# Performance work log

Hardware: AMD Instinct MI355X
Metric: run time of the kernel (lower is better)

## Reference

```python
import jax, jax.numpy as jnp
import numpy as np

E, TOPK, HID, FFN = 8, 2, 1024, 2048  # experts, top_k, hidden K, intermediate N
B, S = 2, 1024


def setup_inputs() -> dict:
    key = jax.random.key(0)
    ks = jax.random.split(key, 7)
    return {
        "x": jax.random.normal(ks[0], (B, S, HID), jnp.float32),
        "router_weight": jax.random.normal(ks[1], (E, HID), jnp.float32) * 0.02,
        "router_bias": jax.random.normal(ks[2], (E,), jnp.float32) * 0.02,
        "w1": jax.random.normal(ks[3], (E, 2 * FFN, HID), jnp.float32) * 0.02,  # [E,2N,K] gate|up
        "w1_bias": jax.random.normal(ks[4], (E, 2 * FFN), jnp.float32) * 0.02,
        "w2": jax.random.normal(ks[5], (E, HID, FFN), jnp.float32) * 0.02,      # [E,K,N]
        "w2_bias": jax.random.normal(ks[6], (E, HID), jnp.float32) * 0.02,
        "top_k": TOPK,
    }


def reference(x, router_weight, router_bias, w1, w1_bias, w2, w2_bias, top_k):
    Bb, Ss, K = x.shape
    xf = x.reshape(-1, K)                                   # [M,K]
    M = xf.shape[0]
    Ne = w1.shape[0]
    # --- route_tokens: softmax over experts, then top-k (megablocks style) ---
    logits = xf @ router_weight.T + router_bias             # [M,E]
    probs = jax.nn.softmax(logits, axis=-1)
    topk_w, topk_ids = jax.lax.top_k(probs, top_k)          # [M,topk]
    # combine weights: scatter top-k probs into dense [M,E]
    comb = jnp.zeros((M, Ne), xf.dtype).at[jnp.arange(M)[:, None], topk_ids].add(topk_w)
    # --- fused experts (dense combine formulation, same math as grouped GEMM) ---
    gu = jnp.einsum('mk,enk->men', xf, w1) + w1_bias[None]  # [M,E,2N]
    Nf = gu.shape[-1] // 2
    gate, up = gu[..., :Nf], gu[..., Nf:]
    h = jax.nn.silu(gate) * up                              # silu_and_mul (SwiGLU)
    down = jnp.einsum('men,ekn->mek', h, w2) + w2_bias[None]  # [M,E,K]
    out = jnp.einsum('mek,me->mk', down, comb)              # weighted combine
    return out.reshape(Bb, Ss, K), topk_w
```

## Files before the change

kernel.cpp:

```cpp
#include <hip/hip_runtime.h>
#include <hip/hip_bf16.h>
#include <math.h>

#define E_    8
#define HID_  1024
#define FFN_  2048
#define M_    2048
#define NP_   (M_*2)

typedef __attribute__((ext_vector_type(8))) short bf16x8;
typedef __attribute__((ext_vector_type(4))) float f32x4;

typedef const __attribute__((address_space(1))) void GVOID;
typedef __attribute__((address_space(3))) void LVOID;

#define VMCNT4 asm volatile("s_waitcnt vmcnt(4)" ::: "memory")
#define VMCNT0 asm volatile("s_waitcnt vmcnt(0)" ::: "memory")

__device__ __forceinline__ short f2bf(float f) {
    union { __hip_bfloat16 b; short s; } u;
    u.b = __float2bfloat16(f);
    return u.s;
}

__global__ __launch_bounds__(256) void cvt_kernel(
    const float* __restrict__ src, __hip_bfloat16* __restrict__ dst, int n4)
{
    int stride = gridDim.x * 256;
    for (int i = blockIdx.x * 256 + threadIdx.x; i < n4; i += stride) {
        float4 v = ((const float4*)src)[i];
        short4 o;
        o.x = f2bf(v.x); o.y = f2bf(v.y); o.z = f2bf(v.z); o.w = f2bf(v.w);
        ((short4*)dst)[i] = o;
    }
}

__global__ __launch_bounds__(64) void router_kernel(
    const float* __restrict__ x, const float* __restrict__ rw,
    const float* __restrict__ rb, int* __restrict__ ids,
    float* __restrict__ wts, int* __restrict__ cnt,
    float* __restrict__ topk_out)
{
    const int m    = blockIdx.x;
    const int lane = threadIdx.x;
    const float4* xm4 = (const float4*)(x + (size_t)m * HID_);

    float4 xv[4];
#pragma unroll
    for (int j = 0; j < 4; ++j) xv[j] = xm4[j*64 + lane];

    float lg[E_];
#pragma unroll
    for (int e = 0; e < E_; ++e) {
        const float4* we4 = (const float4*)(rw + e * HID_);
        float s = 0.f;
#pragma unroll
        for (int j = 0; j < 4; ++j) {
            float4 w = we4[j*64 + lane];
            s = fmaf(xv[j].x, w.x, s);
            s = fmaf(xv[j].y, w.y, s);
            s = fmaf(xv[j].z, w.z, s);
            s = fmaf(xv[j].w, w.w, s);
        }
        lg[e] = s;
    }
#pragma unroll
    for (int off = 32; off; off >>= 1)
#pragma unroll
        for (int e = 0; e < E_; ++e) lg[e] += __shfl_xor(lg[e], off);

    if (lane == 0) {
        float l2[E_], p[E_];
        float mx = -1e30f;
#pragma unroll
        for (int e = 0; e < E_; ++e) { l2[e] = lg[e] + rb[e]; mx = fmaxf(mx, l2[e]); }
        float sum = 0.f;
#pragma unroll
        for (int e = 0; e < E_; ++e) { p[e] = expf(l2[e] - mx); sum += p[e]; }
        float inv = 1.f / sum;
#pragma unroll
        for (int e = 0; e < E_; ++e) p[e] *= inv;

        int   i1 = -1, i2 = -1;
        float v1 = -1e30f, v2 = -1e30f;
#pragma unroll
        for (int e = 0; e < E_; ++e) {
            float pe = p[e];
            if (pe > v1)      { v2 = v1; i2 = i1; v1 = pe; i1 = e; }
            else if (pe > v2) { v2 = pe; i2 = e; }
        }
        ids[2*m]   = i1;  ids[2*m+1]   = i2;
        wts[2*m]   = v1;  wts[2*m+1]   = v2;
        topk_out[2*m]   = v1;
        topk_out[2*m+1] = v2;
        atomicAdd(&cnt[i1], 1);
        atomicAdd(&cnt[i2], 1);
    }
}

__global__ void offsets_kernel(const int* __restrict__ cnt,
                               int* __restrict__ off, int* __restrict__ fill)
{
    if (threadIdx.x == 0 && blockIdx.x == 0) {
        int acc = 0;
        for (int e = 0; e < E_; ++e) { off[e] = acc; fill[e] = acc; acc += cnt[e]; }
    }
}

__global__ __launch_bounds__(256) void scatter_kernel(
    const int* __restrict__ ids, const float* __restrict__ wts,
    int* __restrict__ fill, int* __restrict__ gtok, float* __restrict__ gwt,
    int* __restrict__ pos)
{
    int m = blockIdx.x * 256 + threadIdx.x;
    if (m >= M_) return;
#pragma unroll
    for (int s = 0; s < 2; ++s) {
        int e = ids[2*m + s];
        int p = atomicAdd(&fill[e], 1);
        gtok[p] = m;
        gwt[p]  = wts[2*m + s];
        pos[2*m + s] = p;
    }
}


__global__ __launch_bounds__(256, 3) void gemm1_kernel(
    const __hip_bfloat16* __restrict__ xb, const __hip_bfloat16* __restrict__ w1bf,
    const float* __restrict__ w1b, const int* __restrict__ gtok,
    const int* __restrict__ cnt, const int* __restrict__ off,
    __hip_bfloat16* __restrict__ h)
{
    const int e  = blockIdx.z;
    const int ce = cnt[e];
    const int t0 = blockIdx.y * 128;
    if (t0 >= ce) return;
    const int n0   = blockIdx.x * 64;
    const int base = off[e];
    const __hip_bfloat16* w1e = w1bf + (size_t)e * (2*FFN_) * HID_;

    __shared__ __align__(16) __hip_bfloat16 As[3][128*32];
    __shared__ __align__(16) __hip_bfloat16 Bs[3][128*32];

    const int tid  = threadIdx.x;
    const int lane = tid & 63;
    const int wid  = tid >> 6;
    const int wm   = wid >> 1;
    const int wn   = wid & 1;

    const __hip_bfloat16 *asrc[2], *bsrc[2];
#pragma unroll
    for (int q = 0; q < 2; ++q) {
        int slot = q*256 + tid;
        int r = slot >> 2, p = slot & 3;
        int c = p ^ ((r >> 1) & 3);
        int rr  = min(t0 + r, ce - 1);
        asrc[q] = xb + (size_t)gtok[base + rr] * HID_ + c*8;
        int q2 = r >> 5, s = r & 31;
        int grow = (q2 & 1) ? (FFN_ + n0 + (q2>>1)*32 + s)
                            : (       n0 + (q2>>1)*32 + s);
        bsrc[q] = w1e + (size_t)grow * HID_ + c*8;
    }

    auto STAGE = [&](int b, int k0) {
#pragma unroll
        for (int q = 0; q < 2; ++q)
            __builtin_amdgcn_global_load_lds((GVOID*)(asrc[q] + k0),
                (LVOID*)(&As[b][(q*256 + wid*64)*8]), 16, 0, 0);
#pragma unroll
        for (int q = 0; q < 2; ++q)
            __builtin_amdgcn_global_load_lds((GVOID*)(bsrc[q] + k0),
                (LVOID*)(&Bs[b][(q*256 + wid*64)*8]), 16, 0, 0);
    };

    f32x4 acc[4][4];
#pragma unroll
    for (int m = 0; m < 4; ++m)
#pragma unroll
        for (int n = 0; n < 4; ++n) acc[m][n] = (f32x4){0.f,0.f,0.f,0.f};

    const int cf = lane >> 4;
    auto COMPUTE = [&](int cb) {
        bf16x8 af[4], bfr[4];
#pragma unroll
        for (int m = 0; m < 4; ++m) {
            int r = wm*64 + m*16 + (lane & 15);
            int sw = cf ^ ((r >> 1) & 3);
            af[m] = *(bf16x8*)&As[cb][r*32 + sw*8];
        }
#pragma unroll
        for (int n = 0; n < 4; ++n) {
            int r = wn*64 + n*16 + (lane & 15);
            int sw = cf ^ ((r >> 1) & 3);
            bfr[n] = *(bf16x8*)&Bs[cb][r*32 + sw*8];
        }
        __builtin_amdgcn_s_setprio(1);
#pragma unroll
        for (int m = 0; m < 4; ++m)
#pragma unroll
            for (int n = 0; n < 4; ++n)
                acc[m][n] = __builtin_amdgcn_mfma_f32_16x16x32_bf16(
                    af[m], bfr[n], acc[m][n], 0, 0, 0);
        __builtin_amdgcn_s_setprio(0);
    };

    const int NT = HID_/32;
    STAGE(0, 0);
    STAGE(1, 32);
    VMCNT4;
    __builtin_amdgcn_s_barrier();

    int cb = 0;
    for (int t = 0; t < NT-2; ++t) {
        int sb = cb + 2; if (sb >= 3) sb -= 3;
        STAGE(sb, (t+2)*32);
        COMPUTE(cb);
        VMCNT4;
        __builtin_amdgcn_s_barrier();
        if (++cb == 3) cb = 0;
    }
    COMPUTE(cb);
    VMCNT0;
    __builtin_amdgcn_s_barrier();
    if (++cb == 3) cb = 0;
    COMPUTE(cb);

    const float* w1be = w1b + e*2*FFN_;
#pragma unroll
    for (int n = 0; n < 2; ++n) {
        int col = n0 + wn*32 + n*16 + (lane & 15);
        float bg = w1be[col];
        float bu = w1be[FFN_ + col];
#pragma unroll
        for (int m = 0; m < 4; ++m) {
            int rb2 = t0 + wm*64 + m*16 + (lane >> 4)*4;
#pragma unroll
            for (int i = 0; i < 4; ++i) {
                int t = rb2 + i;
                if (t < ce) {
                    float g = acc[m][n][i]   + bg;
                    float u = acc[m][n+2][i] + bu;
                    float hv = (g / (1.f + __expf(-g))) * u;
                    h[(size_t)(base + t)*FFN_ + col] = __float2bfloat16(hv);
                }
            }
        }
    }
}

__global__ __launch_bounds__(256, 3) void gemm2_kernel(
    const __hip_bfloat16* __restrict__ h, const __hip_bfloat16* __restrict__ w2bf,
    const float* __restrict__ w2b, const float* __restrict__ gwt,
    const int* __restrict__ cnt, const int* __restrict__ off,
    float* __restrict__ dpair)
{
    const int e  = blockIdx.z & 7;
    const int ks = blockIdx.z >> 3;
    const int ce = cnt[e];
    const int t0 = blockIdx.y * 128;
    if (t0 >= ce) return;
    const int n0    = blockIdx.x * 128;
    const int base  = off[e];
    const int kbase = ks * (FFN_/2);
    const __hip_bfloat16* w2e = w2bf + (size_t)e * HID_ * FFN_;

    __shared__ __align__(16) __hip_bfloat16 As[3][128*32];
    __shared__ __align__(16) __hip_bfloat16 Bs[3][128*32];

    const int tid  = threadIdx.x;
    const int lane = tid & 63;
    const int wid  = tid >> 6;
    const int wm   = wid >> 1;
    const int wn   = wid & 1;

    const __hip_bfloat16 *asrc[2], *bsrc[2];
#pragma unroll
    for (int q = 0; q < 2; ++q) {
        int slot = q*256 + tid;
        int r = slot >> 2, p = slot & 3;
        int c = p ^ ((r >> 1) & 3);
        int rr = min(t0 + r, ce - 1);
        asrc[q] = h   + (size_t)(base + rr) * FFN_ + kbase + c*8;
        bsrc[q] = w2e + (size_t)(n0 + r)    * FFN_ + kbase + c*8;
    }

    auto STAGE = [&](int b, int k0) {
#pragma unroll
        for (int q = 0; q < 2; ++q)
            __builtin_amdgcn_global_load_lds((GVOID*)(asrc[q] + k0),
                (LVOID*)(&As[b][(q*256 + wid*64)*8]), 16, 0, 0);
#pragma unroll
        for (int q = 0; q < 2; ++q)
            __builtin_amdgcn_global_load_lds((GVOID*)(bsrc[q] + k0),
                (LVOID*)(&Bs[b][(q*256 + wid*64)*8]), 16, 0, 0);
    };

    f32x4 acc[4][4];
#pragma unroll
    for (int m = 0; m < 4; ++m)
#pragma unroll
        for (int n = 0; n < 4; ++n) acc[m][n] = (f32x4){0.f,0.f,0.f,0.f};

    const int cf = lane >> 4;
    auto COMPUTE = [&](int cb) {
        bf16x8 af[4], bfr[4];
#pragma unroll
        for (int m = 0; m < 4; ++m) {
            int r = wm*64 + m*16 + (lane & 15);
            int sw = cf ^ ((r >> 1) & 3);
            af[m] = *(bf16x8*)&As[cb][r*32 + sw*8];
        }
#pragma unroll
        for (int n = 0; n < 4; ++n) {
            int r = wn*64 + n*16 + (lane & 15);
            int sw = cf ^ ((r >> 1) & 3);
            bfr[n] = *(bf16x8*)&Bs[cb][r*32 + sw*8];
        }
        __builtin_amdgcn_s_setprio(1);
#pragma unroll
        for (int m = 0; m < 4; ++m)
#pragma unroll
            for (int n = 0; n < 4; ++n)
                acc[m][n] = __builtin_amdgcn_mfma_f32_16x16x32_bf16(
                    af[m], bfr[n], acc[m][n], 0, 0, 0);
        __builtin_amdgcn_s_setprio(0);
    };

    const int NT = (FFN_/2)/32;
    STAGE(0, 0);
    STAGE(1, 32);
    VMCNT4;
    __builtin_amdgcn_s_barrier();

    int cb = 0;
    for (int t = 0; t < NT-2; ++t) {
        int sb = cb + 2; if (sb >= 3) sb -= 3;
        STAGE(sb, (t+2)*32);
        COMPUTE(cb);
        VMCNT4;
        __builtin_amdgcn_s_barrier();
        if (++cb == 3) cb = 0;
    }
    COMPUTE(cb);
    VMCNT0;
    __builtin_amdgcn_s_barrier();
    if (++cb == 3) cb = 0;
    COMPUTE(cb);

    const float* w2be = w2b + e*HID_;
    float* dpk = dpair + (size_t)ks * NP_ * HID_;
#pragma unroll
    for (int n = 0; n < 4; ++n) {
        int col = n0 + wn*64 + n*16 + (lane & 15);
        float bias = (ks == 0) ? w2be[col] : 0.f;
#pragma unroll
        for (int m = 0; m < 4; ++m) {
            int rb2 = t0 + wm*64 + m*16 + (lane >> 4)*4;
#pragma unroll
            for (int i = 0; i < 4; ++i) {
                int t = rb2 + i;
                if (t < ce) {
                    int p   = base + t;
                    float w = gwt[p];
                    dpk[(size_t)p*HID_ + col] = w * (acc[m][n][i] + bias);
                }
            }
        }
    }
}

__global__ __launch_bounds__(256) void combine_kernel(
    const float* __restrict__ dpair, const int* __restrict__ pos,
    float* __restrict__ out)
{
    int idx = blockIdx.x * 256 + threadIdx.x;
    int m   = idx >> 8;
    int c4  = (idx & 255) * 4;
    int p0 = pos[2*m], p1 = pos[2*m+1];
    const float* d0 = dpair;
    const float* d1 = dpair + (size_t)NP_ * HID_;
    float4 a0 = *(const float4*)(d0 + (size_t)p0*HID_ + c4);
    float4 a1 = *(const float4*)(d1 + (size_t)p0*HID_ + c4);
    float4 b0 = *(const float4*)(d0 + (size_t)p1*HID_ + c4);
    float4 b1 = *(const float4*)(d1 + (size_t)p1*HID_ + c4);
    float4 o = make_float4((a0.x+a1.x)+(b0.x+b1.x), (a0.y+a1.y)+(b0.y+b1.y),
                           (a0.z+a1.z)+(b0.z+b1.z), (a0.w+a1.w)+(b0.w+b1.w));
    *(float4*)(out + (size_t)m*HID_ + c4) = o;
}

__global__ __launch_bounds__(256) void gemm1_rs_kernel(
    const __hip_bfloat16* __restrict__ xb, const float* __restrict__ w1,
    const float* __restrict__ w1b, const int* __restrict__ gtok,
    const int* __restrict__ cnt, const int* __restrict__ off,
    __hip_bfloat16* __restrict__ h)
{
    const int e  = blockIdx.z;
    const int ce = cnt[e];
    const int t0 = blockIdx.y * 128;
    if (t0 >= ce) return;
    const int n0   = blockIdx.x * 64;
    const int base = off[e];
    const float* w1e = w1 + (size_t)e * (2*FFN_) * HID_;

    __shared__ __align__(16) __hip_bfloat16 As[128*64];
    __shared__ __align__(16) __hip_bfloat16 Bs[128*64];

    const int tid  = threadIdx.x;
    const int lane = tid & 63;
    const int wid  = tid >> 6;
    const int wm   = wid >> 1;
    const int wn   = wid & 1;

    const __hip_bfloat16* asrc[4];
#pragma unroll
    for (int q = 0; q < 4; ++q) {
        int slot = q*256 + tid;
        int r = slot >> 3, p = slot & 7;
        int rr  = min(t0 + r, ce - 1);
        int tok = gtok[base + rr];
        int c = p ^ (r & 7);
        asrc[q] = xb + (size_t)tok * HID_ + c*8;
    }

    const int brow = tid >> 1;
    const int hk   = tid & 1;
    const int q2 = brow >> 5, s = brow & 31;
    const int grow = (q2 & 1) ? (FFN_ + n0 + (q2>>1)*32 + s)
                              : (       n0 + (q2>>1)*32 + s);
    const float* bsrc = w1e + (size_t)grow * HID_ + hk*32;

    f32x4 acc[4][4];
#pragma unroll
    for (int m = 0; m < 4; ++m)
#pragma unroll
        for (int n = 0; n < 4; ++n) acc[m][n] = (f32x4){0.f,0.f,0.f,0.f};

    float4 breg[8];
#pragma unroll
    for (int j = 0; j < 8; ++j) breg[j] = *(const float4*)(bsrc + j*4);

    for (int k0 = 0; k0 < HID_; k0 += 64) {
#pragma unroll
        for (int q = 0; q < 4; ++q) {
            __builtin_amdgcn_global_load_lds(
                (GVOID*)(asrc[q] + k0),
                (LVOID*)(&As[(q*256 + wid*64)*8]), 16, 0, 0);
        }
#pragma unroll
        for (int cc = 0; cc < 4; ++cc) {
            union { bf16x8 v; short s8[8]; } u;
            const float* f0 = (const float*)&breg[2*cc];
#pragma unroll
            for (int j = 0; j < 8; ++j) u.s8[j] = f2bf(f0[j]);
            int c = hk*4 + cc, p = c ^ (brow & 7);
            *(bf16x8*)&Bs[brow*64 + p*8] = u.v;
        }
        __syncthreads();

        if (k0 + 64 < HID_) {
#pragma unroll
            for (int j = 0; j < 8; ++j) breg[j] = *(const float4*)(bsrc + (k0+64) + j*4);
        }

        bf16x8 af[4][2], bfr[4][2];
#pragma unroll
        for (int m = 0; m < 4; ++m)
#pragma unroll
            for (int kk = 0; kk < 2; ++kk) {
                int r = wm*64 + m*16 + (lane & 15);
                int c = kk*4 + (lane >> 4), p = c ^ (r & 7);
                af[m][kk] = *(bf16x8*)&As[r*64 + p*8];
            }
#pragma unroll
        for (int n = 0; n < 4; ++n)
#pragma unroll
            for (int kk = 0; kk < 2; ++kk) {
                int r = wn*64 + n*16 + (lane & 15);
                int c = kk*4 + (lane >> 4), p = c ^ (r & 7);
                bfr[n][kk] = *(bf16x8*)&Bs[r*64 + p*8];
            }
#pragma unroll
        for (int kk = 0; kk < 2; ++kk)
#pragma unroll
            for (int m = 0; m < 4; ++m)
#pragma unroll
                for (int n = 0; n < 4; ++n)
                    acc[m][n] = __builtin_amdgcn_mfma_f32_16x16x32_bf16(
                        af[m][kk], bfr[n][kk], acc[m][n], 0, 0, 0);
        __syncthreads();
    }

    const float* w1be = w1b + e*2*FFN_;
#pragma unroll
    for (int n = 0; n < 2; ++n) {
        int col = n0 + wn*32 + n*16 + (lane & 15);
        float bg = w1be[col];
        float bu = w1be[FFN_ + col];
#pragma unroll
        for (int m = 0; m < 4; ++m) {
            int rb2 = t0 + wm*64 + m*16 + (lane >> 4)*4;
#pragma unroll
            for (int i = 0; i < 4; ++i) {
                int t = rb2 + i;
                if (t < ce) {
                    float g = acc[m][n][i]   + bg;
                    float u = acc[m][n+2][i] + bu;
                    float hv = (g / (1.f + __expf(-g))) * u;
                    h[(size_t)(base + t)*FFN_ + col] = __float2bfloat16(hv);
                }
            }
        }
    }
}

__global__ __launch_bounds__(256) void gemm2_rs_kernel(
    const __hip_bfloat16* __restrict__ h, const float* __restrict__ w2,
    const float* __restrict__ w2b, const int* __restrict__ gtok,
    const float* __restrict__ gwt, const int* __restrict__ cnt,
    const int* __restrict__ off, float* __restrict__ out)
{
    const int e  = blockIdx.z;
    const int ce = cnt[e];
    const int t0 = blockIdx.y * 128;
    if (t0 >= ce) return;
    const int n0   = blockIdx.x * 128;
    const int base = off[e];
    const float* w2e = w2 + (size_t)e * HID_ * FFN_;

    __shared__ __align__(16) __hip_bfloat16 As[128*64];
    __shared__ __align__(16) __hip_bfloat16 Bs[128*64];

    const int tid  = threadIdx.x;
    const int lane = tid & 63;
    const int wid  = tid >> 6;
    const int wm   = wid >> 1;
    const int wn   = wid & 1;

    const __hip_bfloat16* asrc[4];
#pragma unroll
    for (int q = 0; q < 4; ++q) {
        int slot = q*256 + tid;
        int r = slot >> 3, p = slot & 7;
        int rr = min(t0 + r, ce - 1);
        int c = p ^ (r & 7);
        asrc[q] = h + (size_t)(base + rr) * FFN_ + c*8;
    }

    const int brow = tid >> 1;
    const int hk   = tid & 1;
    const float* bsrc = w2e + (size_t)(n0 + brow) * FFN_ + hk*32;

    f32x4 acc[4][4];
#pragma unroll
    for (int m = 0; m < 4; ++m)
#pragma unroll
        for (int n = 0; n < 4; ++n) acc[m][n] = (f32x4){0.f,0.f,0.f,0.f};

    float4 breg[8];
#pragma unroll
    for (int j = 0; j < 8; ++j) breg[j] = *(const float4*)(bsrc + j*4);

    for (int k0 = 0; k0 < FFN_; k0 += 64) {
#pragma unroll
        for (int q = 0; q < 4; ++q) {
            __builtin_amdgcn_global_load_lds(
                (GVOID*)(asrc[q] + k0),
                (LVOID*)(&As[(q*256 + wid*64)*8]), 16, 0, 0);
        }
#pragma unroll
        for (int cc = 0; cc < 4; ++cc) {
            union { bf16x8 v; short s8[8]; } u;
            const float* f0 = (const float*)&breg[2*cc];
#pragma unroll
            for (int j = 0; j < 8; ++j) u.s8[j] = f2bf(f0[j]);
            int c = hk*4 + cc, p = c ^ (brow & 7);
            *(bf16x8*)&Bs[brow*64 + p*8] = u.v;
        }
        __syncthreads();

        if (k0 + 64 < FFN_) {
#pragma unroll
            for (int j = 0; j < 8; ++j) breg[j] = *(const float4*)(bsrc + (k0+64) + j*4);
        }

        bf16x8 af[4][2], bfr[4][2];
#pragma unroll
        for (int m = 0; m < 4; ++m)
#pragma unroll
            for (int kk = 0; kk < 2; ++kk) {
                int r = wm*64 + m*16 + (lane & 15);
                int c = kk*4 + (lane >> 4), p = c ^ (r & 7);
                af[m][kk] = *(bf16x8*)&As[r*64 + p*8];
            }
#pragma unroll
        for (int n = 0; n < 4; ++n)
#pragma unroll
            for (int kk = 0; kk < 2; ++kk) {
                int r = wn*64 + n*16 + (lane & 15);
                int c = kk*4 + (lane >> 4), p = c ^ (r & 7);
                bfr[n][kk] = *(bf16x8*)&Bs[r*64 + p*8];
            }
#pragma unroll
        for (int kk = 0; kk < 2; ++kk)
#pragma unroll
            for (int m = 0; m < 4; ++m)
#pragma unroll
                for (int n = 0; n < 4; ++n)
                    acc[m][n] = __builtin_amdgcn_mfma_f32_16x16x32_bf16(
                        af[m][kk], bfr[n][kk], acc[m][n], 0, 0, 0);
        __syncthreads();
    }

    const float* w2be = w2b + e*HID_;
#pragma unroll
    for (int n = 0; n < 4; ++n) {
        int col = n0 + wn*64 + n*16 + (lane & 15);
        float bias = w2be[col];
#pragma unroll
        for (int m = 0; m < 4; ++m) {
            int rb2 = t0 + wm*64 + m*16 + (lane >> 4)*4;
#pragma unroll
            for (int i = 0; i < 4; ++i) {
                int t = rb2 + i;
                if (t < ce) {
                    int p   = base + t;
                    float w = gwt[p];
                    atomicAdd(&out[(size_t)gtok[p]*HID_ + col], w * (acc[m][n][i] + bias));
                }
            }
        }
    }
}

extern "C" void kernel_launch(void* const* d_in, const int* in_sizes, int n_in,
                              void* d_out, int out_size, void* d_ws, size_t ws_size,
                              hipStream_t stream)
{
    const float* x   = (const float*)d_in[0];
    const float* rw  = (const float*)d_in[1];
    const float* rb  = (const float*)d_in[2];
    const float* w1  = (const float*)d_in[3];
    const float* w1b = (const float*)d_in[4];
    const float* w2  = (const float*)d_in[5];
    const float* w2b = (const float*)d_in[6];

    float* out      = (float*)d_out;
    float* topk_out = out + (size_t)M_ * HID_;

    char*  ws   = (char*)d_ws;
    int*   ids  = (int*)  (ws);
    float* wts  = (float*)(ws + 16384);
    int*   gtok = (int*)  (ws + 32768);
    float* gwt  = (float*)(ws + 49152);
    int*   cnt  = (int*)  (ws + 65536);
    int*   off  = (int*)  (ws + 65536 + 128);
    int*   fill = (int*)  (ws + 65536 + 256);
    int*   pos  = (int*)  (ws + 98304);

    const size_t MB = 1024*1024;
    __hip_bfloat16* xb    = (__hip_bfloat16*)(ws + 131072);
    __hip_bfloat16* h     = (__hip_bfloat16*)(ws + 131072 + 4*MB);
    float*          dpair = (float*)         (ws + 131072 + 20*MB);
    __hip_bfloat16* w1bf  = (__hip_bfloat16*)(ws + 131072 + 52*MB);
    __hip_bfloat16* w2bf  = (__hip_bfloat16*)(ws + 131072 + 116*MB);
    const bool tier2 = (ws_size >= 131072 + 148*MB);

    hipMemsetAsync(cnt, 0, E_ * sizeof(int), stream);

    cvt_kernel<<<2048, 256, 0, stream>>>(x, xb, (M_*HID_)/4);
    router_kernel<<<M_, 64, 0, stream>>>(x, rw, rb, ids, wts, cnt, topk_out);
    offsets_kernel<<<1, 64, 0, stream>>>(cnt, off, fill);
    scatter_kernel<<<M_/256, 256, 0, stream>>>(ids, wts, fill, gtok, gwt, pos);

    if (tier2) {
        cvt_kernel<<<4096, 256, 0, stream>>>(w1, w1bf, (E_*2*FFN_*HID_)/4);
        cvt_kernel<<<4096, 256, 0, stream>>>(w2, w2bf, (E_*HID_*FFN_)/4);

        dim3 g1(FFN_/64, M_/128, E_);
        gemm1_kernel<<<g1, 256, 0, stream>>>(xb, w1bf, w1b, gtok, cnt, off, h);

        dim3 g2(HID_/128, M_/128, 2*E_);
        gemm2_kernel<<<g2, 256, 0, stream>>>(h, w2bf, w2b, gwt, cnt, off, dpair);

        combine_kernel<<<(M_*HID_)/(256*4), 256, 0, stream>>>(dpair, pos, out);
    } else {
        hipMemsetAsync(out, 0, (size_t)M_ * HID_ * sizeof(float), stream);

        dim3 g1(FFN_/64, M_/128, E_);
        gemm1_rs_kernel<<<g1, 256, 0, stream>>>(xb, w1, w1b, gtok, cnt, off, h);

        dim3 g2(HID_/128, M_/128, E_);
        gemm2_rs_kernel<<<g2, 256, 0, stream>>>(h, w2, w2b, gtok, gwt, cnt, off, out);
    }
}
```

Before: 252.2 us.

## Fuse x bf16 conversion into router, merge weight casts, deepen GEMM pipeline

The activation fp32→bf16 conversion moves into the router kernel, which already loads x, so one launch and one read of x go away. The two weight-conversion launches merge into a single kernel. Both grouped GEMMs go from a 3-stage to a 4-stage LDS cp.async ring with vmcnt(8) waits, keeping more loads in flight. In exchange, launch bounds drop to 2 blocks per CU because of the larger shared-memory footprint, which may reduce occupancy.

```diff
diff --git a/kernel.cpp b/kernel.cpp
--- a/kernel.cpp
+++ b/kernel.cpp
@@ -14,6 +14,7 @@
 typedef const __attribute__((address_space(1))) void GVOID;
 typedef __attribute__((address_space(3))) void LVOID;
 
+#define VMCNT8 asm volatile("s_waitcnt vmcnt(8)" ::: "memory")
 #define VMCNT4 asm volatile("s_waitcnt vmcnt(4)" ::: "memory")
 #define VMCNT0 asm volatile("s_waitcnt vmcnt(0)" ::: "memory")
 
@@ -23,15 +24,21 @@
     return u.s;
 }
 
-__global__ __launch_bounds__(256) void cvt_kernel(
-    const float* __restrict__ src, __hip_bfloat16* __restrict__ dst, int n4)
-{
+__global__ __launch_bounds__(256) void cvt_w_kernel(
+    const float* __restrict__ w1, const float* __restrict__ w2,
+    __hip_bfloat16* __restrict__ w1bf, __hip_bfloat16* __restrict__ w2bf)
+{
+    const int n1 = (E_*2*FFN_*HID_)/4;
+    const int n2 = (E_*HID_*FFN_)/4;
     int stride = gridDim.x * 256;
-    for (int i = blockIdx.x * 256 + threadIdx.x; i < n4; i += stride) {
-        float4 v = ((const float4*)src)[i];
+    for (int i = blockIdx.x * 256 + threadIdx.x; i < n1 + n2; i += stride) {
+        float4 v;
+        if (i < n1) v = ((const float4*)w1)[i];
+        else        v = ((const float4*)w2)[i - n1];
         short4 o;
         o.x = f2bf(v.x); o.y = f2bf(v.y); o.z = f2bf(v.z); o.w = f2bf(v.w);
-        ((short4*)dst)[i] = o;
+        if (i < n1) ((short4*)w1bf)[i] = o;
+        else        ((short4*)w2bf)[i - n1] = o;
     }
 }
 
@@ -39,7 +46,7 @@
     const float* __restrict__ x, const float* __restrict__ rw,
     const float* __restrict__ rb, int* __restrict__ ids,
     float* __restrict__ wts, int* __restrict__ cnt,
-    float* __restrict__ topk_out)
+    float* __restrict__ topk_out, __hip_bfloat16* __restrict__ xb)
 {
     const int m    = blockIdx.x;
     const int lane = threadIdx.x;
@@ -48,6 +55,15 @@
     float4 xv[4];
 #pragma unroll
     for (int j = 0; j < 4; ++j) xv[j] = xm4[j*64 + lane];
+
+    short4* xbr = (short4*)(xb + (size_t)m * HID_);
+#pragma unroll
+    for (int j = 0; j < 4; ++j) {
+        short4 o;
+        o.x = f2bf(xv[j].x); o.y = f2bf(xv[j].y);
+        o.z = f2bf(xv[j].z); o.w = f2bf(xv[j].w);
+        xbr[j*64 + lane] = o;
+    }
 
     float lg[E_];
 #pragma unroll
@@ -125,7 +141,7 @@
 }
 
 
-__global__ __launch_bounds__(256, 3) void gemm1_kernel(
+__global__ __launch_bounds__(256, 2) void gemm1_kernel(
     const __hip_bfloat16* __restrict__ xb, const __hip_bfloat16* __restrict__ w1bf,
     const float* __restrict__ w1b, const int* __restrict__ gtok,
     const int* __restrict__ cnt, const int* __restrict__ off,
@@ -139,14 +155,15 @@
     const int base = off[e];
     const __hip_bfloat16* w1e = w1bf + (size_t)e * (2*FFN_) * HID_;
 
-    __shared__ __align__(16) __hip_bfloat16 As[3][128*32];
-    __shared__ __align__(16) __hip_bfloat16 Bs[3][128*32];
+    __shared__ __align__(16) __hip_bfloat16 As[4][128*32];
+    __shared__ __align__(16) __hip_bfloat16 Bs[4][128*32];
 
     const int tid  = threadIdx.x;
     const int lane = tid & 63;
     const int wid  = tid >> 6;
     const int wm   = wid >> 1;
     const int wn   = wid & 1;
+    const int cf   = lane >> 4;
 
     const __hip_bfloat16 *asrc[2], *bsrc[2];
 #pragma unroll
@@ -179,7 +196,6 @@
 #pragma unroll
         for (int n = 0; n < 4; ++n) acc[m][n] = (f32x4){0.f,0.f,0.f,0.f};
 
-    const int cf = lane >> 4;
     auto COMPUTE = [&](int cb) {
         bf16x8 af[4], bfr[4];
 #pragma unroll
@@ -207,23 +223,23 @@
     const int NT = HID_/32;
     STAGE(0, 0);
     STAGE(1, 32);
+    STAGE(2, 64);
+    VMCNT8;
+    __builtin_amdgcn_s_barrier();
+
+    for (int t = 0; t < NT-3; ++t) {
+        STAGE((t+3) & 3, (t+3)*32);
+        COMPUTE(t & 3);
+        VMCNT8;
+        __builtin_amdgcn_s_barrier();
+    }
+    COMPUTE((NT-3) & 3);
     VMCNT4;
     __builtin_amdgcn_s_barrier();
-
-    int cb = 0;
-    for (int t = 0; t < NT-2; ++t) {
-        int sb = cb + 2; if (sb >= 3) sb -= 3;
-        STAGE(sb, (t+2)*32);
-        COMPUTE(cb);
-        VMCNT4;
-        __builtin_amdgcn_s_barrier();
-        if (++cb == 3) cb = 0;
-    }
-    COMPUTE(cb);
+    COMPUTE((NT-2) & 3);
     VMCNT0;
     __builtin_amdgcn_s_barrier();
-    if (++cb == 3) cb = 0;
-    COMPUTE(cb);
+    COMPUTE((NT-1) & 3);
 
     const float* w1be = w1b + e*2*FFN_;
 #pragma unroll
@@ -248,7 +264,7 @@
     }
 }
 
-__global__ __launch_bounds__(256, 3) void gemm2_kernel(
+__global__ __launch_bounds__(256, 2) void gemm2_kernel(
     const __hip_bfloat16* __restrict__ h, const __hip_bfloat16* __restrict__ w2bf,
     const float* __restrict__ w2b, const float* __restrict__ gwt,
     const int* __restrict__ cnt, const int* __restrict__ off,
@@ -264,14 +280,15 @@
     const int kbase = ks * (FFN_/2);
     const __hip_bfloat16* w2e = w2bf + (size_t)e * HID_ * FFN_;
 
-    __shared__ __align__(16) __hip_bfloat16 As[3][128*32];
-    __shared__ __align__(16) __hip_bfloat16 Bs[3][128*32];
+    __shared__ __align__(16) __hip_bfloat16 As[4][128*32];
+    __shared__ __align__(16) __hip_bfloat16 Bs[4][128*32];
 
     const int tid  = threadIdx.x;
     const int lane = tid & 63;
     const int wid  = tid >> 6;
     const int wm   = wid >> 1;
     const int wn   = wid & 1;
+    const int cf   = lane >> 4;
 
     const __hip_bfloat16 *asrc[2], *bsrc[2];
 #pragma unroll
@@ -301,7 +318,6 @@
 #pragma unroll
         for (int n = 0; n < 4; ++n) acc[m][n] = (f32x4){0.f,0.f,0.f,0.f};
 
-    const int cf = lane >> 4;
     auto COMPUTE = [&](int cb) {
         bf16x8 af[4], bfr[4];
 #pragma unroll
@@ -329,23 +345,23 @@
     const int NT = (FFN_/2)/32;
     STAGE(0, 0);
     STAGE(1, 32);
+    STAGE(2, 64);
+    VMCNT8;
+    __builtin_amdgcn_s_barrier();
+
+    for (int t = 0; t < NT-3; ++t) {
+        STAGE((t+3) & 3, (t+3)*32);
+        COMPUTE(t & 3);
+        VMCNT8;
+        __builtin_amdgcn_s_barrier();
+    }
+    COMPUTE((NT-3) & 3);
     VMCNT4;
     __builtin_amdgcn_s_barrier();
-
-    int cb = 0;
-    for (int t = 0; t < NT-2; ++t) {
-        int sb = cb + 2; if (sb >= 3) sb -= 3;
-        STAGE(sb, (t+2)*32);
-        COMPUTE(cb);
-        VMCNT4;
-        __builtin_amdgcn_s_barrier();
-        if (++cb == 3) cb = 0;
-    }
-    COMPUTE(cb);
+    COMPUTE((NT-2) & 3);
     VMCNT0;
     __builtin_amdgcn_s_barrier();
-    if (++cb == 3) cb = 0;
-    COMPUTE(cb);
+    COMPUTE((NT-1) & 3);
 
     const float* w2be = w2b + e*HID_;
     float* dpk = dpair + (size_t)ks * NP_ * HID_;
@@ -667,14 +683,12 @@
 
     hipMemsetAsync(cnt, 0, E_ * sizeof(int), stream);
 
-    cvt_kernel<<<2048, 256, 0, stream>>>(x, xb, (M_*HID_)/4);
-    router_kernel<<<M_, 64, 0, stream>>>(x, rw, rb, ids, wts, cnt, topk_out);
+    router_kernel<<<M_, 64, 0, stream>>>(x, rw, rb, ids, wts, cnt, topk_out, xb);
     offsets_kernel<<<1, 64, 0, stream>>>(cnt, off, fill);
     scatter_kernel<<<M_/256, 256, 0, stream>>>(ids, wts, fill, gtok, gwt, pos);
 
     if (tier2) {
-        cvt_kernel<<<4096, 256, 0, stream>>>(w1, w1bf, (E_*2*FFN_*HID_)/4);
-        cvt_kernel<<<4096, 256, 0, stream>>>(w2, w2bf, (E_*HID_*FFN_)/4);
+        cvt_w_kernel<<<4096, 256, 0, stream>>>(w1, w2, w1bf, w2bf);
 
         dim3 g1(FFN_/64, M_/128, E_);
         gemm1_kernel<<<g1, 256, 0, stream>>>(xb, w1bf, w1b, gtok, cnt, off, h);
```

Measured after the change: 287.0 us. 13.8% more time.
